# Kernel optimization log

Hardware: AMD Instinct MI355X
Metric: run time of the kernel (lower is better)

The kernel has to match this reference:

```python
import jax, jax.numpy as jnp
import numpy as np
from jax import lax

N = 4667      # num vertices (hardcoded in Spatial_Attention_layer)
B = 4         # batch
T = 8         # raw timesteps; (T-2)*3 == 18 after TimeBlock + concat
C_IN = 2      # input features
TP = 18       # concatenated timesteps
HID = 16      # TimeBlock out channels / PCN fc width
N_ROOTS = 500
BRANCH = 2
DEPTH = 3


def _build_tree():
    # Static stand-in for the P/roots/s2rDic dict-based trajectory tree.
    rng = np.random.RandomState(42)
    roots = rng.choice(N, N_ROOTS, replace=False)
    path_node = [int(r) for r in roots]
    levels = []
    prev = list(range(N_ROOTS))
    for _ in range(DEPTH):
        p_idx, c_idx, pn, cn, nxt = [], [], [], [], []
        for pi in prev:
            kids = rng.choice(N, BRANCH, replace=False)
            for c in kids:
                ci = len(path_node)
                path_node.append(int(c))
                p_idx.append(pi); c_idx.append(ci)
                pn.append(path_node[pi]); cn.append(int(c))
                nxt.append(ci)
        levels.append((np.array(p_idx), np.array(c_idx), np.array(pn), np.array(cn)))
        prev = nxt
    leaf_idx = np.array(prev)
    leaf_node = np.array([path_node[i] for i in prev])
    return np.asarray(roots), levels, leaf_idx, leaf_node, len(path_node)

ROOTS, LEVELS, LEAF_IDX, LEAF_NODES, NUM_PATHS = _build_tree()
ROOT_PATH_IDX = np.arange(N_ROOTS)


def setup_inputs() -> dict:
    key = jax.random.key(0)
    ks = jax.random.split(key, 16)
    f = jnp.float32
    rn = lambda k, s: 0.1 * jax.random.normal(k, s, f)
    return {
        "X": jax.random.normal(ks[0], (B, N, T, C_IN), f),
        "X_daily": jax.random.normal(ks[1], (B, N, T, C_IN), f),
        "X_weekly": jax.random.normal(ks[2], (B, N, T, C_IN), f),
        "mask": jnp.zeros((1,), jnp.int32),  # unused in forward (as in source)
        "conv1_w": rn(ks[3], (HID, C_IN, 1, 3)),
        "conv1_b": rn(ks[4], (HID,)),
        "conv2_w": rn(ks[5], (HID, C_IN, 1, 3)),
        "conv2_b": rn(ks[6], (HID,)),
        "W1": rn(ks[7], (HID,)),
        "W2": rn(ks[8], (TP, HID)),
        "W3": rn(ks[9], (TP,)),
        "bs": rn(ks[10], (1, N, N)),
        "Vs": rn(ks[11], (N, N)),
        "fc_w": rn(ks[12], (HID, HID)),
        "fc_b": rn(ks[13], (HID,)),
    }


def reference(X, X_daily, X_weekly, mask, conv1_w, conv1_b, conv2_w, conv2_b,
              W1, W2, W3, bs, Vs, fc_w, fc_b):
    dn = ("NCHW", "OIHW", "NCHW")

    def time_block(Xin):
        # [B,N,T,C] -> [B,C,N,T] -> GLU conv over time -> [B,N,T-2,HID]
        Xp = jnp.transpose(Xin, (0, 3, 1, 2))
        c1 = lax.conv_general_dilated(Xp, conv1_w, (1, 1), "VALID", dimension_numbers=dn) + conv1_b[None, :, None, None]
        c2 = lax.conv_general_dilated(Xp, conv2_w, (1, 1), "VALID", dimension_numbers=dn) + conv2_b[None, :, None, None]
        return jnp.transpose(c1 * jax.nn.sigmoid(c2), (0, 2, 3, 1))

    x = jnp.concatenate([time_block(X), time_block(X_daily), time_block(X_weekly)], axis=2)  # [B,N,18,16]

    # spatial attention
    lhs = jnp.einsum("bnt,tc->bnc", jnp.einsum("bntc,c->bnt", x, W1), W2)   # [B,N,16]
    rhs = jnp.einsum("t,bntc->bnc", W3, x)                                    # [B,N,16]
    product = jnp.einsum("bnc,bmc->bnm", lhs, rhs)                            # [B,N,N]
    S = jnp.einsum("nm,bmk->bnk", Vs, jax.nn.sigmoid(product + bs))           # [B,N,N]
    A = jax.nn.softmax(S, axis=1)

    # PCN tree propagation: h_child = fc(h_parent) * A[:, p, c] + x[c]
    xn = jnp.transpose(x, (1, 0, 2, 3))  # [N,B,18,16]
    H = jnp.zeros((NUM_PATHS, B, TP, HID), x.dtype)
    H = H.at[ROOT_PATH_IDX].set(xn[ROOTS])
    for p_idx, c_idx, pn, cn in LEVELS:
        hp = H[p_idx]                                   # [E,B,18,16]
        a = jnp.transpose(A[:, pn, cn])                 # [E,B]
        hc = (jnp.einsum("ebtc,dc->ebtd", hp, fc_w) + fc_b) * a[:, :, None, None] + xn[cn]
        H = H.at[c_idx].set(hc)

    # mean-pool leaf paths per terminal node; fall back to x for nodes w/o leaves
    leaf_h = H[LEAF_IDX]
    sums = jax.ops.segment_sum(leaf_h, LEAF_NODES, num_segments=N)
    counts = jax.ops.segment_sum(jnp.ones((LEAF_NODES.shape[0],), x.dtype), LEAF_NODES, num_segments=N)
    has_leaf = (counts > 0)[:, None, None, None]
    out_n = jnp.where(has_leaf, sums / jnp.maximum(counts, 1.0)[:, None, None, None], xn)
    return jnp.transpose(out_n, (1, 0, 2, 3))  # [B,N,18,16]
```

## Files before the change

kernel.cpp:

```cpp
#include <hip/hip_runtime.h>
#include <stdint.h>
#include <string.h>

#define NV      4667
#define BB      4
#define TT      8
#define TPX     18
#define HID     16
#define NROOTS  500
#define NPATHS  7500
#define NEDGES  7000
#define NLEAF   4000
#define NP2     4864
#define LDKQ    5120
#define NSIGM   20
#define NSIGK   76

typedef __bf16 bf16;
typedef bf16  bf16x4 __attribute__((ext_vector_type(4)));
typedef int   i32x4v __attribute__((ext_vector_type(4)));
typedef const void __attribute__((address_space(1))) gvoid;
typedef void       __attribute__((address_space(3))) svoid;

struct MT19937 {
    uint32_t mt[624]; int pos;
    void seed(uint32_t s) {
        for (int i = 0; i < 624; ++i) { mt[i] = s; s = 1812433253u * (s ^ (s >> 30)) + (uint32_t)i + 1u; }
        pos = 624;
    }
    uint32_t next() {
        if (pos >= 624) {
            for (int i = 0; i < 624; ++i) {
                uint32_t y = (mt[i] & 0x80000000u) | (mt[(i + 1) % 624] & 0x7fffffffu);
                uint32_t v = mt[(i + 397) % 624] ^ (y >> 1);
                if (y & 1u) v ^= 0x9908b0dfu;
                mt[i] = v;
            }
            pos = 0;
        }
        uint32_t y = mt[pos++];
        y ^= y >> 11; y ^= (y << 7) & 0x9d2c5680u; y ^= (y << 15) & 0xefc60000u; y ^= y >> 18;
        return y;
    }
    uint32_t interval(uint32_t mx) {
        if (!mx) return 0;
        uint32_t mask = mx;
        mask |= mask >> 1; mask |= mask >> 2; mask |= mask >> 4; mask |= mask >> 8; mask |= mask >> 16;
        uint32_t v;
        do { v = next() & mask; } while (v > mx);
        return v;
    }
};

struct TreeBlob {
    int path_node[NPATHS];
    int leaf_start[NV + 1];
    int leaf_path[NLEAF];
};

static void build_tree_host(TreeBlob* tb) {
    MT19937 rng; rng.seed(42);
    static int perm[NV];
    auto choice_take = [&](int* out, int k) {
        for (int i = 0; i < NV; ++i) perm[i] = i;
        for (int i = NV - 1; i >= 1; --i) {
            int j = (int)rng.interval((uint32_t)i);
            int t = perm[i]; perm[i] = perm[j]; perm[j] = t;
        }
        for (int i = 0; i < k; ++i) out[i] = perm[i];
    };
    int np_ = 0;
    int roots[NROOTS];
    choice_take(roots, NROOTS);
    for (int i = 0; i < NROOTS; ++i) tb->path_node[np_++] = roots[i];
    int prev_cnt = NROOTS;
    for (int lvl = 0; lvl < 3; ++lvl) {
        int kids[2];
        for (int p = 0; p < prev_cnt; ++p) {
            choice_take(kids, 2);
            tb->path_node[np_++] = kids[0];
            tb->path_node[np_++] = kids[1];
        }
        prev_cnt *= 2;
    }
    static int cnt[NV], cur[NV];
    memset(cnt, 0, sizeof(cnt));
    for (int l = 0; l < NLEAF; ++l) cnt[tb->path_node[3500 + l]]++;
    tb->leaf_start[0] = 0;
    for (int n = 0; n < NV; ++n) tb->leaf_start[n + 1] = tb->leaf_start[n] + cnt[n];
    for (int n = 0; n < NV; ++n) cur[n] = tb->leaf_start[n];
    for (int l = 0; l < NLEAF; ++l) {
        int n = tb->path_node[3500 + l];
        tb->leaf_path[cur[n]++] = 3500 + l;
    }
}

static TreeBlob* get_pinned_tree() {
    static TreeBlob* p = [] {
        TreeBlob* q = nullptr;
        if (hipHostMalloc((void**)&q, sizeof(TreeBlob), 0) != hipSuccess || !q) {
            static TreeBlob fallback;
            q = &fallback;
        }
        build_tree_host(q);
        return q;
    }();
    return p;
}

__global__ void k_timeblock(const float* __restrict__ X, const float* __restrict__ Xd,
                            const float* __restrict__ Xw,
                            const float* __restrict__ w1, const float* __restrict__ b1,
                            const float* __restrict__ w2, const float* __restrict__ b2,
                            float* __restrict__ x) {
    int idx = blockIdx.x * 256 + threadIdx.x;
    if (idx >= BB * NV * 18) return;
    int t = idx % 6;
    int g = (idx / 6) % 3;
    int n = (idx / 18) % NV;
    int b = idx / (18 * NV);
    const float* Xg = (g == 0) ? X : (g == 1) ? Xd : Xw;
    const float* p = Xg + (((size_t)b * NV + n) * TT + t) * 2;
    float v[6];
#pragma unroll
    for (int kk = 0; kk < 3; ++kk) { v[kk * 2 + 0] = p[kk * 2 + 0]; v[kk * 2 + 1] = p[kk * 2 + 1]; }
    float* xo = x + (((size_t)b * NV + n) * TPX + (g * 6 + t)) * HID;
#pragma unroll
    for (int o = 0; o < 16; ++o) {
        float c1 = b1[o], c2 = b2[o];
#pragma unroll
        for (int ci = 0; ci < 2; ++ci)
#pragma unroll
            for (int kk = 0; kk < 3; ++kk) {
                float xv = v[kk * 2 + ci];
                c1 += xv * w1[(o * 2 + ci) * 3 + kk];
                c2 += xv * w2[(o * 2 + ci) * 3 + kk];
            }
        xo[o] = c1 * (1.0f / (1.0f + __expf(-c2)));
    }
}

__global__ void k_lhsrhs(const float* __restrict__ x, const float* __restrict__ W1,
                         const float* __restrict__ W2, const float* __restrict__ W3,
                         float* __restrict__ lhs, float* __restrict__ rhs) {
    int idx = blockIdx.x * 256 + threadIdx.x;
    if (idx >= BB * NV) return;
    const float* xp = x + (size_t)idx * TPX * HID;
    float l[16], r[16];
#pragma unroll
    for (int c = 0; c < 16; ++c) { l[c] = 0.f; r[c] = 0.f; }
    for (int t = 0; t < TPX; ++t) {
        float xt = 0.f, w3 = W3[t];
#pragma unroll
        for (int c = 0; c < 16; ++c) { float xv = xp[t * 16 + c]; xt += xv * W1[c]; r[c] += w3 * xv; }
#pragma unroll
        for (int c = 0; c < 16; ++c) l[c] += xt * W2[t * 16 + c];
    }
    float* lo = lhs + (size_t)idx * 16;
    float* ro = rhs + (size_t)idx * 16;
#pragma unroll
    for (int c = 0; c < 16; ++c) { lo[c] = l[c]; ro[c] = r[c]; }
}

__global__ __launch_bounds__(256)
void k_prep(const float* __restrict__ Vs, int8_t* __restrict__ Vq,
            float* __restrict__ sA, float* __restrict__ c0,
            const float* __restrict__ lhs, const float* __restrict__ rhs,
            const float* __restrict__ bs, int8_t* __restrict__ Sq,
            float* __restrict__ colsum) {
    __shared__ float wred[4];
    __shared__ int ired[4];
    __shared__ bf16 bss[64 * 260];
    int blk = blockIdx.x;
    int t = threadIdx.x;

    if (blk < NP2) {
        if (blk < 19) {
#pragma unroll
            for (int u = 0; u < 4; ++u) {
                int ii = blk * 1024 + u * 256 + t;
                if (ii < BB * NV) colsum[ii] = 0.f;
            }
        }
        int n = blk;
        int8_t* row_out = Vq + (size_t)n * LDKQ;
        if (n >= NV) {
            for (int m = t * 4; m < LDKQ; m += 1024) *(int*)(row_out + m) = 0;
            if (t == 0) { sA[n] = 0.f; c0[n] = 0.f; }
            return;
        }
        const float* row = Vs + (size_t)n * NV;
        float v[20];
        float mx = 0.f;
#pragma unroll
        for (int i = 0; i < 20; ++i) {
            int m = t + i * 256;
            v[i] = (m < NV) ? row[m] : 0.f;
            mx = fmaxf(mx, fabsf(v[i]));
        }
#pragma unroll
        for (int o = 32; o; o >>= 1) mx = fmaxf(mx, __shfl_xor(mx, o));
        if ((t & 63) == 0) wred[t >> 6] = mx;
        __syncthreads();
        mx = fmaxf(fmaxf(wred[0], wred[1]), fmaxf(wred[2], wred[3]));
        mx = fmaxf(mx, 1e-30f);
        float inv = 127.f / mx;
        int qs = 0;
#pragma unroll
        for (int i = 0; i < 20; ++i) {
            int q = (int)rintf(v[i] * inv);
            qs += q;
            row_out[t + i * 256] = (int8_t)q;
        }
#pragma unroll
        for (int o = 32; o; o >>= 1) qs += __shfl_xor(qs, o);
        if ((t & 63) == 0) ired[t >> 6] = qs;
        __syncthreads();
        if (t == 0) {
            int tot = ired[0] + ired[1] + ired[2] + ired[3];
            sA[n] = mx / 32258.f;
            c0[n] = mx * (float)tot / 254.f;
        }
        return;
    }

    int bid = blk - NP2;
    int m0 = (bid % NSIGM) * 256;
    int k0 = (bid / NSIGM) * 64;

    for (int i = t; i < 256 * 64; i += 256) {
        int row = i >> 6, col = i & 63;
        int mg = m0 + row, kg = k0 + col;
        float v = (mg < NV && kg < NV) ? bs[(size_t)mg * NV + kg] : 0.f;
        bss[col * 260 + row] = (bf16)v;
    }
    __syncthreads();

    int ml = t & 63, kc = t >> 6;
    int mbase = m0 + ml * 4;

    for (int b = 0; b < BB; ++b) {
        float lv[4][16];
#pragma unroll
        for (int r = 0; r < 4; ++r) {
            int mg = mbase + r;
            if (mg < NV) {
                const float4* lp = (const float4*)&lhs[((size_t)b * NV + mg) * 16];
#pragma unroll
                for (int q = 0; q < 4; ++q) {
                    float4 f = lp[q];
                    lv[r][q * 4 + 0] = f.x; lv[r][q * 4 + 1] = f.y;
                    lv[r][q * 4 + 2] = f.z; lv[r][q * 4 + 3] = f.w;
                }
            } else {
#pragma unroll
                for (int c = 0; c < 16; ++c) lv[r][c] = 0.f;
            }
        }
#pragma unroll
        for (int kk = 0; kk < 16; ++kk) {
            int kl = kc * 16 + kk;
            int kg = k0 + kl;
            bool kvalid = (kg < NV);
            float rsv[16];
            if (kvalid) {
                const float4* rp = (const float4*)&rhs[((size_t)b * NV + kg) * 16];
#pragma unroll
                for (int q = 0; q < 4; ++q) {
                    float4 f = rp[q];
                    rsv[q * 4 + 0] = f.x; rsv[q * 4 + 1] = f.y;
                    rsv[q * 4 + 2] = f.z; rsv[q * 4 + 3] = f.w;
                }
            } else {
#pragma unroll
                for (int c = 0; c < 16; ++c) rsv[c] = 0.f;
            }
            bf16x4 bv = *(const bf16x4*)&bss[kl * 260 + ml * 4];
            int pack = 0;
#pragma unroll
            for (int r = 0; r < 4; ++r) {
                float dot = 0.f;
#pragma unroll
                for (int c = 0; c < 16; ++c) dot += lv[r][c] * rsv[c];
                float pv = dot + (float)bv[r];
                float s = 1.0f / (1.0f + __expf(-pv));
                int q = 0;
                if (kvalid && (mbase + r) < NV) q = (int)rintf(254.f * (s - 0.5f));
                pack |= (q & 0xff) << (8 * r);
            }
            *(int*)&Sq[((size_t)b * NP2 + kg) * LDKQ + mbase] = pack;
        }
    }
}

#define BUF1 65536

#define STAGE8(BUF, kt) { \
    const int8_t* _ga = gA + (size_t)(kt) * 128; \
    const int8_t* _gb = gB + (size_t)(kt) * 128; \
    __builtin_amdgcn_global_load_lds((gvoid*)(_ga),                      (svoid*)(ldsb + (BUF) + dst0), 16, 0, 0); \
    __builtin_amdgcn_global_load_lds((gvoid*)(_ga + (size_t)64  * LDKQ), (svoid*)(ldsb + (BUF) + dst0 + 8192), 16, 0, 0); \
    __builtin_amdgcn_global_load_lds((gvoid*)(_ga + (size_t)128 * LDKQ), (svoid*)(ldsb + (BUF) + dst0 + 16384), 16, 0, 0); \
    __builtin_amdgcn_global_load_lds((gvoid*)(_ga + (size_t)192 * LDKQ), (svoid*)(ldsb + (BUF) + dst0 + 24576), 16, 0, 0); \
    __builtin_amdgcn_global_load_lds((gvoid*)(_gb),                      (svoid*)(ldsb + (BUF) + 32768 + dst0), 16, 0, 0); \
    __builtin_amdgcn_global_load_lds((gvoid*)(_gb + (size_t)64  * LDKQ), (svoid*)(ldsb + (BUF) + 32768 + dst0 + 8192), 16, 0, 0); \
    __builtin_amdgcn_global_load_lds((gvoid*)(_gb + (size_t)128 * LDKQ), (svoid*)(ldsb + (BUF) + 32768 + dst0 + 16384), 16, 0, 0); \
    __builtin_amdgcn_global_load_lds((gvoid*)(_gb + (size_t)192 * LDKQ), (svoid*)(ldsb + (BUF) + 32768 + dst0 + 24576), 16, 0, 0); }

#define RD(BUF, KS) { \
    _Pragma("unroll") for (int mf = 0; mf < 8; ++mf) \
        af[mf] = *(const i32x4v*)(ldsb + (BUF) + arow + mf * 2048 + ck[KS]); \
    _Pragma("unroll") for (int nj = 0; nj < 4; ++nj) \
        bf[nj] = *(const i32x4v*)(ldsb + (BUF) + brow + nj * 2048 + ck[KS]); }

#define MM() { \
    __builtin_amdgcn_s_setprio(1); \
    _Pragma("unroll") for (int mf = 0; mf < 8; ++mf) \
    _Pragma("unroll") for (int nj = 0; nj < 4; ++nj) \
        acc[mf][nj] = __builtin_amdgcn_mfma_i32_16x16x64_i8(af[mf], bf[nj], acc[mf][nj], 0, 0, 0); \
    __builtin_amdgcn_s_setprio(0); }

__global__ __launch_bounds__(512, 2)
void k_gemm16(const int8_t* __restrict__ Vq, const int8_t* __restrict__ Sq,
              const float* __restrict__ sA, const float* __restrict__ c0,
              float* __restrict__ colsum) {
    extern __shared__ char ldsb[];

    int orig = blockIdx.x;
    int xcd = orig & 7, lin = orig >> 3;
    int wg = (xcd < 4) ? xcd * 181 + lin : 724 + (xcd - 4) * 180 + lin;
    int bi = wg % 19;
    int bk = (wg / 19) % 19;
    int bb = wg / 361;

    int t = threadIdx.x;
    int lane = t & 63, wv = t >> 6;
    int wr = wv >> 2, wc = wv & 3;
    int lr = lane & 15, lg = lane >> 4;
    int key = (lr & 7) << 4;

    int ck[2];
    ck[0] = (lg * 16) ^ key;
    ck[1] = (64 + lg * 16) ^ key;
    int arow = wr * 16384 + lr * 128;
    int brow = 32768 + wc * 8192 + lr * 128;

    int rl0 = t >> 3;
    int csw = ((t & 7) << 4) ^ ((rl0 & 7) << 4);
    const int8_t* gA = Vq + ((size_t)(bi * 256) + rl0) * LDKQ + csw;
    const int8_t* gB = Sq + ((size_t)bb * NP2 + (size_t)bk * 256 + rl0) * LDKQ + csw;
    int dst0 = t * 16;

    i32x4v acc[8][4];
#pragma unroll
    for (int i = 0; i < 8; ++i)
#pragma unroll
        for (int j = 0; j < 4; ++j) acc[i][j] = i32x4v{0, 0, 0, 0};

    i32x4v af[8], bf[4];

    STAGE8(0, 0);
    asm volatile("s_waitcnt vmcnt(0)" ::: "memory");
    __builtin_amdgcn_s_barrier();

    for (int ti = 0; ti < 38; ++ti) {
        int cur = (ti & 1) ? BUF1 : 0;
        int nxt = cur ^ BUF1;
        STAGE8(nxt, ti + 1);
        RD(cur, 0);
        MM();
        RD(cur, 1);
        MM();
        asm volatile("s_waitcnt vmcnt(0)" ::: "memory");
        __builtin_amdgcn_s_barrier();
    }

#pragma unroll
    for (int nj = 0; nj < 4; ++nj) {
        int col = bk * 256 + wc * 64 + nj * 16 + lr;
        float csum = 0.f;
#pragma unroll
        for (int mf = 0; mf < 8; ++mf) {
            int rowb = bi * 256 + wr * 128 + mf * 16 + lg * 4;
            float4 sa4 = *(const float4*)&sA[rowb];
            float4 c04 = *(const float4*)&c0[rowb];
            float sar[4] = {sa4.x, sa4.y, sa4.z, sa4.w};
            float c0r[4] = {c04.x, c04.y, c04.z, c04.w};
#pragma unroll
            for (int r = 0; r < 4; ++r) {
                float S = sar[r] * (float)acc[mf][nj][r] + c0r[r];
                csum += ((rowb + r) < NV && col < NV) ? __expf(S) : 0.f;
            }
        }
        csum += __shfl_xor(csum, 16);
        csum += __shfl_xor(csum, 32);
        if (lane < 16 && col < NV) atomicAdd(&colsum[(size_t)bb * NV + col], csum);
    }
}

__global__ void k_edge(const int8_t* __restrict__ Vq, const int8_t* __restrict__ Sq,
                       const float* __restrict__ sA, const float* __restrict__ c0,
                       const float* __restrict__ colsum, const int* __restrict__ path_node,
                       float* __restrict__ a_edge) {
    int g = blockIdx.x;
    int b = threadIdx.x >> 6;
    int lane = threadIdx.x & 63;
    int e, pbase, cbase;
    if (g < 1000)      { e = g;        pbase = 0;    cbase = 500;  }
    else if (g < 3000) { e = g - 1000; pbase = 500;  cbase = 1500; }
    else               { e = g - 3000; pbase = 1500; cbase = 3500; }
    int pn = path_node[pbase + (e >> 1)];
    int cn = path_node[cbase + e];
    const int8_t* va = Vq + (size_t)pn * LDKQ;
    const int8_t* vb = Sq + ((size_t)b * NP2 + cn) * LDKQ;
    int acc = 0;
    for (int i = lane * 16; i < LDKQ; i += 1024) {
        i32x4v a4 = *(const i32x4v*)(va + i);
        i32x4v b4 = *(const i32x4v*)(vb + i);
#pragma unroll
        for (int w = 0; w < 4; ++w) {
            int aw = a4[w], bw = b4[w];
#pragma unroll
            for (int q = 0; q < 4; ++q)
                acc += (int)(int8_t)(aw >> (8 * q)) * (int)(int8_t)(bw >> (8 * q));
        }
    }
#pragma unroll
    for (int o = 32; o; o >>= 1) acc += __shfl_xor(acc, o);
    if (lane == 0) {
        float S = sA[pn] * (float)acc + c0[pn];
        a_edge[(size_t)g * BB + b] = __expf(S) / colsum[(size_t)b * NV + cn];
    }
}

__global__ __launch_bounds__(256)
void k_level(const float* __restrict__ x, const int* __restrict__ path_node,
             const float* __restrict__ fcw, const float* __restrict__ fcb,
             const float* __restrict__ a_edge, float* __restrict__ H,
             int E, int pbase, int cbase, int gbase, int lvl1) {
    int idx = blockIdx.x * 256 + threadIdx.x;
    if (idx >= E * BB * TPX) return;
    int t = idx % TPX;
    int b = (idx / TPX) & 3;
    int e = idx / (TPX * BB);
    int pp = pbase + (e >> 1);
    const float* hp;
    if (lvl1) {
        int pn = path_node[pp];
        hp = &x[(((size_t)b * NV + pn) * TPX + t) * HID];
    } else {
        hp = &H[(((size_t)pp * BB + b) * TPX + t) * HID];
    }
    float h[16];
    const float4* hp4 = (const float4*)hp;
#pragma unroll
    for (int q = 0; q < 4; ++q) {
        float4 f = hp4[q];
        h[q * 4 + 0] = f.x; h[q * 4 + 1] = f.y; h[q * 4 + 2] = f.z; h[q * 4 + 3] = f.w;
    }
    float a = a_edge[(size_t)(gbase + e) * BB + b];
    int cp = cbase + e;
    int cn = path_node[cp];
    const float4* xv4 = (const float4*)&x[(((size_t)b * NV + cn) * TPX + t) * HID];
    float4* outp = (float4*)&H[(((size_t)cp * BB + b) * TPX + t) * HID];
#pragma unroll
    for (int q = 0; q < 4; ++q) {
        float4 xv = xv4[q];
        float o[4];
#pragma unroll
        for (int j = 0; j < 4; ++j) {
            int d = q * 4 + j;
            float acc = fcb[d];
#pragma unroll
            for (int c = 0; c < 16; ++c) acc += h[c] * fcw[d * 16 + c];
            o[j] = acc * a;
        }
        float4 ov; ov.x = o[0] + xv.x; ov.y = o[1] + xv.y; ov.z = o[2] + xv.z; ov.w = o[3] + xv.w;
        outp[q] = ov;
    }
}

__global__ void k_pool(const float* __restrict__ x, const float* __restrict__ H,
                       const int* __restrict__ leaf_start, const int* __restrict__ leaf_path,
                       float* __restrict__ out) {
    int n = blockIdx.x;
    int s = leaf_start[n], epos = leaf_start[n + 1];
    int cnt = epos - s;
    for (int idx = threadIdx.x; idx < BB * 288; idx += 256) {
        int b = idx / 288, d = idx % 288;
        float v;
        if (cnt == 0) {
            v = x[((size_t)b * NV + n) * 288 + d];
        } else {
            float sum = 0.f;
            for (int l = s; l < epos; ++l) {
                int p = leaf_path[l];
                sum += H[((size_t)p * BB + b) * 288 + d];
            }
            v = sum / (float)cnt;
        }
        out[((size_t)b * NV + n) * 288 + d] = v;
    }
}

extern "C" void kernel_launch(void* const* d_in, const int* in_sizes, int n_in,
                              void* d_out, int out_size, void* d_ws, size_t ws_size,
                              hipStream_t stream) {
    const float* X   = (const float*)d_in[0];
    const float* Xd  = (const float*)d_in[1];
    const float* Xw  = (const float*)d_in[2];
    const float* c1w = (const float*)d_in[4];
    const float* c1b = (const float*)d_in[5];
    const float* c2w = (const float*)d_in[6];
    const float* c2b = (const float*)d_in[7];
    const float* W1  = (const float*)d_in[8];
    const float* W2  = (const float*)d_in[9];
    const float* W3  = (const float*)d_in[10];
    const float* bs  = (const float*)d_in[11];
    const float* Vs  = (const float*)d_in[12];
    const float* fcw = (const float*)d_in[13];
    const float* fcb = (const float*)d_in[14];
    float* out = (float*)d_out;

    TreeBlob* pinned = get_pinned_tree();

    char* w = (char*)d_ws;
    auto alloc = [&](size_t bytes) { char* p = w; w += (bytes + 255) & ~(size_t)255; return p; };
    float*  x      = (float*)alloc((size_t)BB * NV * 288 * 4);
    float*  lhs    = (float*)alloc((size_t)BB * NV * 16 * 4);
    float*  rhs    = (float*)alloc((size_t)BB * NV * 16 * 4);
    float*  colsum = (float*)alloc((size_t)BB * NV * 4);
    float*  aedge  = (float*)alloc((size_t)NEDGES * BB * 4);
    float*  H      = (float*)alloc((size_t)NPATHS * BB * 288 * 4);
    float*  sAr    = (float*)alloc((size_t)NP2 * 4);
    float*  c0r    = (float*)alloc((size_t)NP2 * 4);
    int*    dtree  = (int*)alloc(sizeof(TreeBlob));
    int8_t* Vq     = (int8_t*)alloc((size_t)NP2 * LDKQ);
    int8_t* Sq     = (int8_t*)alloc((size_t)BB * NP2 * LDKQ);

    int* d_path   = dtree;
    int* d_lstart = dtree + NPATHS;
    int* d_lpath  = d_lstart + (NV + 1);

    hipFuncSetAttribute((const void*)k_gemm16, hipFuncAttributeMaxDynamicSharedMemorySize, 131072);

    hipMemcpyAsync(dtree, pinned, sizeof(TreeBlob), hipMemcpyHostToDevice, stream);

    k_timeblock<<<(BB * NV * 18 + 255) / 256, 256, 0, stream>>>(X, Xd, Xw, c1w, c1b, c2w, c2b, x);
    k_lhsrhs<<<(BB * NV + 255) / 256, 256, 0, stream>>>(x, W1, W2, W3, lhs, rhs);
    k_prep<<<NP2 + NSIGM * NSIGK, 256, 0, stream>>>(Vs, Vq, sAr, c0r, lhs, rhs, bs, Sq, colsum);
    k_gemm16<<<19 * 19 * BB, 512, 131072, stream>>>(Vq, Sq, sAr, c0r, colsum);
    k_edge<<<NEDGES, 256, 0, stream>>>(Vq, Sq, sAr, c0r, colsum, d_path, aedge);
    k_level<<<(1000 * BB * TPX + 255) / 256, 256, 0, stream>>>(x, d_path, fcw, fcb, aedge, H, 1000, 0, 500, 0, 1);
    k_level<<<(2000 * BB * TPX + 255) / 256, 256, 0, stream>>>(x, d_path, fcw, fcb, aedge, H, 2000, 500, 1500, 1000, 0);
    k_level<<<(4000 * BB * TPX + 255) / 256, 256, 0, stream>>>(x, d_path, fcw, fcb, aedge, H, 4000, 1500, 3500, 3000, 0);
    k_pool<<<NV, 256, 0, stream>>>(x, H, d_lstart, d_lpath, out);
}
```

Baseline: 725.8 us.

## Deepen int8 GEMM pipeline to four 64-wide K stages with partial vmcnt waits

Result: no change. 740.2 us (+2.0%).

```diff
diff --git a/kernel.cpp b/kernel.cpp
--- a/kernel.cpp
+++ b/kernel.cpp
@@ -293,25 +293,24 @@
     }
 }
 
-#define BUF1 65536
-
-#define STAGE8(BUF, kt) { \
-    const int8_t* _ga = gA + (size_t)(kt) * 128; \
-    const int8_t* _gb = gB + (size_t)(kt) * 128; \
+#define RB0 0
+#define RB1 32768
+#define RB2 65536
+#define RB3 98304
+
+#define STAGE4(BUF, kt) { \
+    const int8_t* _ga = gA + (size_t)(kt) * 64; \
+    const int8_t* _gb = gB + (size_t)(kt) * 64; \
     __builtin_amdgcn_global_load_lds((gvoid*)(_ga),                      (svoid*)(ldsb + (BUF) + dst0), 16, 0, 0); \
-    __builtin_amdgcn_global_load_lds((gvoid*)(_ga + (size_t)64  * LDKQ), (svoid*)(ldsb + (BUF) + dst0 + 8192), 16, 0, 0); \
-    __builtin_amdgcn_global_load_lds((gvoid*)(_ga + (size_t)128 * LDKQ), (svoid*)(ldsb + (BUF) + dst0 + 16384), 16, 0, 0); \
-    __builtin_amdgcn_global_load_lds((gvoid*)(_ga + (size_t)192 * LDKQ), (svoid*)(ldsb + (BUF) + dst0 + 24576), 16, 0, 0); \
-    __builtin_amdgcn_global_load_lds((gvoid*)(_gb),                      (svoid*)(ldsb + (BUF) + 32768 + dst0), 16, 0, 0); \
-    __builtin_amdgcn_global_load_lds((gvoid*)(_gb + (size_t)64  * LDKQ), (svoid*)(ldsb + (BUF) + 32768 + dst0 + 8192), 16, 0, 0); \
-    __builtin_amdgcn_global_load_lds((gvoid*)(_gb + (size_t)128 * LDKQ), (svoid*)(ldsb + (BUF) + 32768 + dst0 + 16384), 16, 0, 0); \
-    __builtin_amdgcn_global_load_lds((gvoid*)(_gb + (size_t)192 * LDKQ), (svoid*)(ldsb + (BUF) + 32768 + dst0 + 24576), 16, 0, 0); }
-
-#define RD(BUF, KS) { \
+    __builtin_amdgcn_global_load_lds((gvoid*)(_ga + (size_t)128 * LDKQ), (svoid*)(ldsb + (BUF) + dst0 + 8192), 16, 0, 0); \
+    __builtin_amdgcn_global_load_lds((gvoid*)(_gb),                      (svoid*)(ldsb + (BUF) + dst0 + 16384), 16, 0, 0); \
+    __builtin_amdgcn_global_load_lds((gvoid*)(_gb + (size_t)128 * LDKQ), (svoid*)(ldsb + (BUF) + dst0 + 24576), 16, 0, 0); }
+
+#define RD(BUF) { \
     _Pragma("unroll") for (int mf = 0; mf < 8; ++mf) \
-        af[mf] = *(const i32x4v*)(ldsb + (BUF) + arow + mf * 2048 + ck[KS]); \
+        af[mf] = *(const i32x4v*)(ldsb + (BUF) + arow + mf * 1024); \
     _Pragma("unroll") for (int nj = 0; nj < 4; ++nj) \
-        bf[nj] = *(const i32x4v*)(ldsb + (BUF) + brow + nj * 2048 + ck[KS]); }
+        bf[nj] = *(const i32x4v*)(ldsb + (BUF) + brow + nj * 1024); }
 
 #define MM() { \
     __builtin_amdgcn_s_setprio(1); \
@@ -320,8 +319,15 @@
         acc[mf][nj] = __builtin_amdgcn_mfma_i32_16x16x64_i8(af[mf], bf[nj], acc[mf][nj], 0, 0, 0); \
     __builtin_amdgcn_s_setprio(0); }
 
+#define WIN(CUR, STG, kt) { \
+    STAGE4(STG, kt); \
+    RD(CUR); \
+    MM(); \
+    asm volatile("s_waitcnt vmcnt(8)" ::: "memory"); \
+    __builtin_amdgcn_s_barrier(); }
+
 __global__ __launch_bounds__(512, 2)
-void k_gemm16(const int8_t* __restrict__ Vq, const int8_t* __restrict__ Sq,
+void k_gemm64(const int8_t* __restrict__ Vq, const int8_t* __restrict__ Sq,
               const float* __restrict__ sA, const float* __restrict__ c0,
               float* __restrict__ colsum) {
     extern __shared__ char ldsb[];
@@ -337,16 +343,13 @@
     int lane = t & 63, wv = t >> 6;
     int wr = wv >> 2, wc = wv & 3;
     int lr = lane & 15, lg = lane >> 4;
-    int key = (lr & 7) << 4;
-
-    int ck[2];
-    ck[0] = (lg * 16) ^ key;
-    ck[1] = (64 + lg * 16) ^ key;
-    int arow = wr * 16384 + lr * 128;
-    int brow = 32768 + wc * 8192 + lr * 128;
-
-    int rl0 = t >> 3;
-    int csw = ((t & 7) << 4) ^ ((rl0 & 7) << 4);
+
+    int ck = (lg * 16) ^ (((lr >> 2) & 3) << 4);
+    int arow = wr * 8192 + lr * 64 + ck;
+    int brow = 16384 + wc * 4096 + lr * 64 + ck;
+
+    int rl0 = t >> 2;
+    int csw = ((t & 3) << 4) ^ (((t >> 4) & 3) << 4);
     const int8_t* gA = Vq + ((size_t)(bi * 256) + rl0) * LDKQ + csw;
     const int8_t* gB = Sq + ((size_t)bb * NP2 + (size_t)bk * 256 + rl0) * LDKQ + csw;
     int dst0 = t * 16;
@@ -359,21 +362,21 @@
 
     i32x4v af[8], bf[4];
 
-    STAGE8(0, 0);
+    STAGE4(RB0, 0);
+    STAGE4(RB1, 1);
+    STAGE4(RB2, 2);
+    asm volatile("s_waitcnt vmcnt(8)" ::: "memory");
+    __builtin_amdgcn_s_barrier();
+
+    for (int q = 0; q < 18; ++q) {
+        WIN(RB0, RB3, 4 * q + 3);
+        WIN(RB1, RB0, 4 * q + 4);
+        WIN(RB2, RB1, 4 * q + 5);
+        WIN(RB3, RB2, 4 * q + 6);
+    }
+    WIN(RB0, RB3, 75);
+    WIN(RB1, RB0, 76);
     asm volatile("s_waitcnt vmcnt(0)" ::: "memory");
-    __builtin_amdgcn_s_barrier();
-
-    for (int ti = 0; ti < 38; ++ti) {
-        int cur = (ti & 1) ? BUF1 : 0;
-        int nxt = cur ^ BUF1;
-        STAGE8(nxt, ti + 1);
-        RD(cur, 0);
-        MM();
-        RD(cur, 1);
-        MM();
-        asm volatile("s_waitcnt vmcnt(0)" ::: "memory");
-        __builtin_amdgcn_s_barrier();
-    }
 
 #pragma unroll
     for (int nj = 0; nj < 4; ++nj) {
@@ -542,14 +545,14 @@
     int* d_lstart = dtree + NPATHS;
     int* d_lpath  = d_lstart + (NV + 1);
 
-    hipFuncSetAttribute((const void*)k_gemm16, hipFuncAttributeMaxDynamicSharedMemorySize, 131072);
+    hipFuncSetAttribute((const void*)k_gemm64, hipFuncAttributeMaxDynamicSharedMemorySize, 131072);
 
     hipMemcpyAsync(dtree, pinned, sizeof(TreeBlob), hipMemcpyHostToDevice, stream);
 
     k_timeblock<<<(BB * NV * 18 + 255) / 256, 256, 0, stream>>>(X, Xd, Xw, c1w, c1b, c2w, c2b, x);
     k_lhsrhs<<<(BB * NV + 255) / 256, 256, 0, stream>>>(x, W1, W2, W3, lhs, rhs);
     k_prep<<<NP2 + NSIGM * NSIGK, 256, 0, stream>>>(Vs, Vq, sAr, c0r, lhs, rhs, bs, Sq, colsum);
-    k_gemm16<<<19 * 19 * BB, 512, 131072, stream>>>(Vq, Sq, sAr, c0r, colsum);
+    k_gemm64<<<19 * 19 * BB, 512, 131072, stream>>>(Vq, Sq, sAr, c0r, colsum);
     k_edge<<<NEDGES, 256, 0, stream>>>(Vq, Sq, sAr, c0r, colsum, d_path, aedge);
     k_level<<<(1000 * BB * TPX + 255) / 256, 256, 0, stream>>>(x, d_path, fcw, fcb, aedge, H, 1000, 0, 500, 0, 1);
     k_level<<<(2000 * BB * TPX + 255) / 256, 256, 0, stream>>>(x, d_path, fcw, fcb, aedge, H, 2000, 500, 1500, 1000, 0);
```
